# Kernel optimization log

Hardware: AMD Instinct MI355X
Metric: run time of the kernel (lower is better)

## Reference

```python
import jax, jax.numpy as jnp
import numpy as np

N = 50000       # nodes per layer
L = 2           # multiplex layers
F_IN = 128
F_OUT = 32
E_L = 800000    # in-layer edges per layer
NEG_SLOPE = 0.2  # LeakyReLU(0.2)


def _merge_edges(edges_per_layer):
    # offset each layer's edges into the global L*N index space
    parts = [edges_per_layer[i] + i * N for i in range(L)]
    all_edges = jnp.concatenate(parts, axis=1)
    dt = all_edges.dtype
    # self loops on every (layer, node)
    self_loops = jnp.tile(jnp.arange(L * N, dtype=dt)[None, :], (2, 1))
    all_edges = jnp.concatenate([all_edges, self_loops], axis=1)
    # interlayer loops: torch.combinations(arange(L), r=2) + flip([0,1])
    pairs = np.array([(i, j) for i in range(L) for j in range(i + 1, L)], dtype=np.int64)
    pairs = np.concatenate([pairs, pairs[::-1, ::-1]], axis=0)
    all_nodes = np.arange(L * N, dtype=np.int64).reshape(L, N)
    src = all_nodes[pairs[:, 0]].reshape(-1)
    trg = all_nodes[pairs[:, 1]].reshape(-1)
    inter = jnp.asarray(np.stack([src, trg], axis=0)).astype(dt)
    return jnp.concatenate([all_edges, inter], axis=1)  # [2, E_total]


def setup_inputs() -> dict:
    key = jax.random.key(0)
    k1, k2, k3, k4, k5 = jax.random.split(key, 5)
    return {
        "x": jax.random.normal(k1, (1, N, F_IN), dtype=jnp.float32),
        "edge_index0": jax.random.randint(k2, (2, E_L), 0, N, dtype=jnp.int32),
        "edge_index1": jax.random.randint(k3, (2, E_L), 0, N, dtype=jnp.int32),
        "W_proj": jax.random.normal(k4, (L * F_OUT, F_IN), dtype=jnp.float32) * 0.05,
        "W_merge": jax.random.normal(k5, (F_OUT, L * F_OUT), dtype=jnp.float32) * 0.05,
        "bias": jnp.zeros((L, F_OUT), dtype=jnp.float32),
    }


def reference(x, edge_index0, edge_index1, W_proj, W_merge, bias):
    # dropout_prob=0 -> dropout is identity (eval-mode semantics)
    B = x.shape[0]
    edges = _merge_edges([edge_index0, edge_index1])
    src, trg = edges[0], edges[1]
    # degree normalization (naming follows original: in_deg from src, out_deg from trg)
    in_deg = 1.0 / jnp.sqrt(jnp.zeros(L * N, x.dtype).at[src].add(1.0))
    out_deg = 1.0 / jnp.sqrt(jnp.zeros(L * N, x.dtype).at[trg].add(1.0))
    # project F_IN -> L*F_OUT, then split features into L chunks concatenated on node dim
    proj = jnp.einsum('bnf,of->bno', x, W_proj)                 # [B, N, L*F_OUT]
    proj = proj.reshape(B, N, L, F_OUT).transpose(0, 2, 1, 3).reshape(B, L * N, F_OUT)
    proj = proj * out_deg[None, :, None]
    lifted = proj[:, src, :]                                    # [B, E, F_OUT] gather
    agg = jnp.zeros((B, L * N, F_OUT), x.dtype).at[:, trg, :].add(lifted)  # scatter_add
    agg = agg * in_deg[None, :, None]
    out = agg.reshape(B, L, N, F_OUT).transpose(0, 2, 1, 3)     # [B, N, L, F_OUT]
    out = jax.nn.leaky_relu(out + bias, NEG_SLOPE)
    return jnp.einsum('bnk,ok->bno', out.reshape(B, N, L * F_OUT), W_merge)  # [B, N, F_OUT]
```

## Files before the change

kernel.cpp:

```cpp
#include <hip/hip_runtime.h>

#define N_NODES 50000
#define F_IN 128
#define F_OUT 32
#define E_L 800000
#define NEG_SLOPE 0.2f
#define LN 100000
#define NE 1600000
#define BSH 6
#define BNODES 64
#define NB 782
#define CAP 2368
#define PBLOCKS 512
#define PCHUNK 3125
#define CEDGE 7

__global__ __launch_bounds__(512) void partition_kernel(
    const int* __restrict__ e0, const int* __restrict__ e1,
    int* __restrict__ cur_t, int* __restrict__ cur_s,
    int* __restrict__ trgbuf, unsigned char* __restrict__ srcbuf) {
    __shared__ int hist_t[NB], hist_s[NB], res_t[NB], res_s[NB];
    const int t = threadIdx.x, b = blockIdx.x;
    const int l = (b >= PBLOCKS / 2) ? 1 : 0;
    const int* __restrict__ ei = l ? e1 : e0;
    const int ebase = b * PCHUNK - l * E_L;
    for (int i = t; i < NB; i += 512) { hist_t[i] = 0; hist_s[i] = 0; }
    __syncthreads();
    int cs_[CEDGE], ct_[CEDGE];
    #pragma unroll
    for (int j = 0; j < CEDGE; ++j) {
        const int idx = t + j * 512;
        if (idx < PCHUNK) {
            const int e = ebase + idx;
            const int src = ei[e], trg = ei[E_L + e];
            cs_[j] = src; ct_[j] = trg;
            atomicAdd(&hist_t[trg >> BSH], 1);
            atomicAdd(&hist_s[src >> BSH], 1);
        } else { cs_[j] = -1; ct_[j] = -1; }
    }
    __syncthreads();
    for (int i = t; i < NB; i += 512) {
        res_t[i] = hist_t[i] ? atomicAdd(&cur_t[i], hist_t[i]) : 0;
        res_s[i] = hist_s[i] ? atomicAdd(&cur_s[i], hist_s[i]) : 0;
    }
    __syncthreads();
    for (int i = t; i < NB; i += 512) { hist_t[i] = 0; hist_s[i] = 0; }
    __syncthreads();
    #pragma unroll
    for (int j = 0; j < CEDGE; ++j) {
        if (ct_[j] >= 0) {
            const int src = cs_[j], trg = ct_[j];
            const int tb = trg >> BSH, sb = src >> BSH;
            const int st = res_t[tb] + atomicAdd(&hist_t[tb], 1);
            const int ss = res_s[sb] + atomicAdd(&hist_s[sb], 1);
            if (st < CAP)
                trgbuf[tb * CAP + st] =
                    (((l << 6) | (trg & 63)) << 17) | (src + l * N_NODES);
            if (ss < CAP)
                srcbuf[sb * CAP + ss] = (unsigned char)((l << 6) | (src & 63));
        }
    }
}

__global__ __launch_bounds__(256) void count_kernel(
    const int* __restrict__ cur_t, const int* __restrict__ cur_s,
    const int* __restrict__ trgbuf, const unsigned char* __restrict__ srcbuf,
    int* __restrict__ cnt_trg, int* __restrict__ cnt_src) {
    __shared__ int ht[128], hs[128];
    const int t = threadIdx.x, b = blockIdx.x;
    if (t < 128) { ht[t] = 0; hs[t] = 0; }
    __syncthreads();
    const int ct = min(cur_t[b], CAP), cs = min(cur_s[b], CAP);
    for (int i = t; i < ct; i += 256)
        atomicAdd(&ht[(trgbuf[b * CAP + i] >> 17) & 127], 1);
    for (int i = t; i < cs; i += 256)
        atomicAdd(&hs[srcbuf[b * CAP + i] & 127], 1);
    __syncthreads();
    if (t < 128) {
        const int l = t >> 6, n = b * BNODES + (t & 63);
        if (n < N_NODES) {
            cnt_trg[l * N_NODES + n] = ht[t];
            cnt_src[l * N_NODES + n] = hs[t];
        }
    }
}

__global__ __launch_bounds__(256) void proj_kernel(
    const float* __restrict__ x, const float* __restrict__ Wp,
    const int* __restrict__ cnt_trg, float* __restrict__ scaled) {
    __shared__ float Wtt[64][132];
    __shared__ float xt[8][F_IN];
    const int t = threadIdx.x;
    for (int i = t; i < 64 * F_IN; i += 256) {
        int o = i >> 7, k = i & 127;
        Wtt[o][k] = Wp[i];
    }
    const int lane = t & 63, w = t >> 6;
    const int ntiles = N_NODES / 8;
    for (int tile = blockIdx.x; tile < ntiles; tile += gridDim.x) {
        const int base = tile * 8;
        __syncthreads();
        ((float4*)&xt[0][0])[t] = ((const float4*)(x + (size_t)base * F_IN))[t];
        __syncthreads();
        const int n0 = w, n1 = w + 4;
        float acc0 = 0.f, acc1 = 0.f;
        #pragma unroll
        for (int k = 0; k < F_IN; k += 4) {
            float4 wv = *(const float4*)&Wtt[lane][k];
            float4 x0 = *(const float4*)&xt[n0][k];
            float4 x1 = *(const float4*)&xt[n1][k];
            acc0 += wv.x * x0.x + wv.y * x0.y + wv.z * x0.z + wv.w * x0.w;
            acc1 += wv.x * x1.x + wv.y * x1.y + wv.z * x1.z + wv.w * x1.w;
        }
        const int l = lane >> 5, f = lane & 31;
        {
            const int v = l * N_NODES + base + n0;
            const float od = 1.0f / sqrtf((float)(cnt_trg[v] + 2));
            scaled[(size_t)v * F_OUT + f] = acc0 * od;
        }
        {
            const int v = l * N_NODES + base + n1;
            const float od = 1.0f / sqrtf((float)(cnt_trg[v] + 2));
            scaled[(size_t)v * F_OUT + f] = acc1 * od;
        }
    }
}

__global__ __launch_bounds__(512) void mega_kernel(
    const int* __restrict__ cur_t, const int* __restrict__ trgbuf,
    const int* __restrict__ cnt_trg, const int* __restrict__ cnt_src,
    const float* __restrict__ scaled, const float* __restrict__ Wm,
    const float* __restrict__ bias, float* __restrict__ out) {
    __shared__ int   colx[CAP];
    __shared__ int   rp[128], rdeg[128], cursor[128], sc[128];
    __shared__ float h[BNODES][64];
    __shared__ float Wt[64][32];
    __shared__ float bs[64];
    const int t = threadIdx.x, b = blockIdx.x;
    for (int i = t; i < 2048; i += 512) Wt[i >> 5][i & 31] = Wm[(i & 31) * 64 + (i >> 5)];
    if (t < 64) bs[t] = bias[t];
    int cnt_r = 0;
    if (t < 128) {
        const int l = t >> 6, n = b * BNODES + (t & 63);
        cnt_r = (n < N_NODES) ? cnt_trg[l * N_NODES + n] : 0;
        rdeg[t] = cnt_r; sc[t] = cnt_r;
    }
    __syncthreads();
    for (int off = 1; off < 128; off <<= 1) {
        int add = (t < 128 && t >= off) ? sc[t - off] : 0;
        __syncthreads();
        if (t < 128) sc[t] += add;
        __syncthreads();
    }
    if (t < 128) { rp[t] = sc[t] - cnt_r; cursor[t] = sc[t] - cnt_r; }
    __syncthreads();
    const int total = min(cur_t[b], CAP);
    for (int i = t; i < total; i += 512) {
        const int p = trgbuf[b * CAP + i];
        const int slot = atomicAdd(&cursor[(p >> 17) & 127], 1);
        colx[slot] = p & 0x1FFFF;
    }
    __syncthreads();
    const int nl = t >> 3, f = (t & 7) * 4;
    const int n = b * BNODES + nl;
    if (n < N_NODES) {
        const int s0 = rp[nl],      d0 = rdeg[nl];
        const int s1 = rp[nl + 64], d1 = rdeg[nl + 64];
        float4 acc0 = make_float4(0.f, 0.f, 0.f, 0.f);
        float4 acc1 = make_float4(0.f, 0.f, 0.f, 0.f);
        const int m = (d0 > d1) ? d0 : d1;
        #pragma unroll 2
        for (int i = 0; i < m; ++i) {
            if (i < d0) {
                const int u = colx[s0 + i];
                const float4 g = *(const float4*)(scaled + (size_t)u * F_OUT + f);
                acc0.x += g.x; acc0.y += g.y; acc0.z += g.z; acc0.w += g.w;
            }
            if (i < d1) {
                const int u = colx[s1 + i];
                const float4 g = *(const float4*)(scaled + (size_t)u * F_OUT + f);
                acc1.x += g.x; acc1.y += g.y; acc1.z += g.z; acc1.w += g.w;
            }
        }
        const int v = n, vp = N_NODES + n;
        const float4 sv = *(const float4*)(scaled + (size_t)v  * F_OUT + f);
        const float4 pv = *(const float4*)(scaled + (size_t)vp * F_OUT + f);
        const float id0 = rsqrtf((float)(cnt_src[v]  + 2));
        const float id1 = rsqrtf((float)(cnt_src[vp] + 2));
        float4 h0, h1;
        h0.x = (acc0.x + sv.x + pv.x) * id0 + bs[f + 0];
        h0.y = (acc0.y + sv.y + pv.y) * id0 + bs[f + 1];
        h0.z = (acc0.z + sv.z + pv.z) * id0 + bs[f + 2];
        h0.w = (acc0.w + sv.w + pv.w) * id0 + bs[f + 3];
        h1.x = (acc1.x + sv.x + pv.x) * id1 + bs[32 + f + 0];
        h1.y = (acc1.y + sv.y + pv.y) * id1 + bs[32 + f + 1];
        h1.z = (acc1.z + sv.z + pv.z) * id1 + bs[32 + f + 2];
        h1.w = (acc1.w + sv.w + pv.w) * id1 + bs[32 + f + 3];
        h0.x = (h0.x >= 0.f) ? h0.x : NEG_SLOPE * h0.x;
        h0.y = (h0.y >= 0.f) ? h0.y : NEG_SLOPE * h0.y;
        h0.z = (h0.z >= 0.f) ? h0.z : NEG_SLOPE * h0.z;
        h0.w = (h0.w >= 0.f) ? h0.w : NEG_SLOPE * h0.w;
        h1.x = (h1.x >= 0.f) ? h1.x : NEG_SLOPE * h1.x;
        h1.y = (h1.y >= 0.f) ? h1.y : NEG_SLOPE * h1.y;
        h1.z = (h1.z >= 0.f) ? h1.z : NEG_SLOPE * h1.z;
        h1.w = (h1.w >= 0.f) ? h1.w : NEG_SLOPE * h1.w;
        *(float4*)&h[nl][f]      = h0;
        *(float4*)&h[nl][32 + f] = h1;
    }
    __syncthreads();
    for (int i = t; i < BNODES * 32; i += 512) {
        const int nl2 = i >> 5, o = i & 31, n2 = b * BNODES + nl2;
        if (n2 < N_NODES) {
            float acc = 0.f;
            #pragma unroll
            for (int k = 0; k < 64; ++k)
                acc += h[nl2][k] * Wt[k][o];
            out[(size_t)n2 * F_OUT + o] = acc;
        }
    }
}

extern "C" void kernel_launch(void* const* d_in, const int* in_sizes, int n_in,
                              void* d_out, int out_size, void* d_ws, size_t ws_size,
                              hipStream_t stream) {
    const float* x    = (const float*)d_in[0];
    const int*   e0   = (const int*)d_in[1];
    const int*   e1   = (const int*)d_in[2];
    const float* Wp   = (const float*)d_in[3];
    const float* Wm   = (const float*)d_in[4];
    const float* bias = (const float*)d_in[5];
    float* out = (float*)d_out;

    float* scaled = (float*)d_ws;
    unsigned char* srcbuf = (unsigned char*)d_ws;
    int* trgbuf  = (int*)((char*)d_ws + (size_t)LN * F_OUT * sizeof(float));
    int* cur_t   = trgbuf + (size_t)NB * CAP;
    int* cur_s   = cur_t + NB;
    int* cnt_trg = cur_s + NB;
    int* cnt_src = cnt_trg + LN;

    hipMemsetAsync(cur_t, 0, 2 * NB * sizeof(int), stream);

    partition_kernel<<<PBLOCKS, 512, 0, stream>>>(e0, e1, cur_t, cur_s,
                                                  trgbuf, srcbuf);
    count_kernel<<<NB, 256, 0, stream>>>(cur_t, cur_s, trgbuf, srcbuf,
                                         cnt_trg, cnt_src);
    proj_kernel<<<1024, 256, 0, stream>>>(x, Wp, cnt_trg, scaled);
    mega_kernel<<<NB, 512, 0, stream>>>(cur_t, trgbuf, cnt_trg, cnt_src,
                                        scaled, Wm, bias, out);
}
```

Before: 203.3 us.

## Fold degree counting into partition via global atomics and drop count kernel

Removes the separate count kernel and the source-side bucketing buffer. Per-node in/out degrees are now counted directly in the partition kernel with global atomicAdds, and the within-block slot offset from the first histogram pass is reused, so the second shared-atomic pass goes away. The partition grid is halved so each block handles twice the edges. This trades a kernel launch and extra buffer traffic for 3.2M scattered global atomics and a larger memset.

```diff
diff --git a/kernel.cpp b/kernel.cpp
--- a/kernel.cpp
+++ b/kernel.cpp
@@ -11,76 +11,46 @@
 #define BNODES 64
 #define NB 782
 #define CAP 2368
-#define PBLOCKS 512
-#define PCHUNK 3125
-#define CEDGE 7
+#define PBLOCKS 256
+#define PCHUNK 6250
+#define CEDGE 13
 
 __global__ __launch_bounds__(512) void partition_kernel(
     const int* __restrict__ e0, const int* __restrict__ e1,
-    int* __restrict__ cur_t, int* __restrict__ cur_s,
-    int* __restrict__ trgbuf, unsigned char* __restrict__ srcbuf) {
-    __shared__ int hist_t[NB], hist_s[NB], res_t[NB], res_s[NB];
+    int* __restrict__ cur_t, int* __restrict__ trgbuf,
+    int* __restrict__ cnt_trg, int* __restrict__ cnt_src) {
+    __shared__ int hist_t[NB], res_t[NB];
     const int t = threadIdx.x, b = blockIdx.x;
     const int l = (b >= PBLOCKS / 2) ? 1 : 0;
     const int* __restrict__ ei = l ? e1 : e0;
     const int ebase = b * PCHUNK - l * E_L;
-    for (int i = t; i < NB; i += 512) { hist_t[i] = 0; hist_s[i] = 0; }
-    __syncthreads();
-    int cs_[CEDGE], ct_[CEDGE];
+    for (int i = t; i < NB; i += 512) hist_t[i] = 0;
+    __syncthreads();
+    int cu_[CEDGE], ct_[CEDGE], off_[CEDGE];
     #pragma unroll
     for (int j = 0; j < CEDGE; ++j) {
         const int idx = t + j * 512;
         if (idx < PCHUNK) {
             const int e = ebase + idx;
             const int src = ei[e], trg = ei[E_L + e];
-            cs_[j] = src; ct_[j] = trg;
-            atomicAdd(&hist_t[trg >> BSH], 1);
-            atomicAdd(&hist_s[src >> BSH], 1);
-        } else { cs_[j] = -1; ct_[j] = -1; }
-    }
-    __syncthreads();
-    for (int i = t; i < NB; i += 512) {
+            cu_[j] = src; ct_[j] = trg;
+            off_[j] = atomicAdd(&hist_t[trg >> BSH], 1);
+            atomicAdd(&cnt_trg[l * N_NODES + trg], 1);
+            atomicAdd(&cnt_src[l * N_NODES + src], 1);
+        } else { ct_[j] = -1; off_[j] = 0; cu_[j] = 0; }
+    }
+    __syncthreads();
+    for (int i = t; i < NB; i += 512)
         res_t[i] = hist_t[i] ? atomicAdd(&cur_t[i], hist_t[i]) : 0;
-        res_s[i] = hist_s[i] ? atomicAdd(&cur_s[i], hist_s[i]) : 0;
-    }
-    __syncthreads();
-    for (int i = t; i < NB; i += 512) { hist_t[i] = 0; hist_s[i] = 0; }
     __syncthreads();
     #pragma unroll
     for (int j = 0; j < CEDGE; ++j) {
         if (ct_[j] >= 0) {
-            const int src = cs_[j], trg = ct_[j];
-            const int tb = trg >> BSH, sb = src >> BSH;
-            const int st = res_t[tb] + atomicAdd(&hist_t[tb], 1);
-            const int ss = res_s[sb] + atomicAdd(&hist_s[sb], 1);
+            const int trg = ct_[j], tb = trg >> BSH;
+            const int st = res_t[tb] + off_[j];
             if (st < CAP)
                 trgbuf[tb * CAP + st] =
-                    (((l << 6) | (trg & 63)) << 17) | (src + l * N_NODES);
-            if (ss < CAP)
-                srcbuf[sb * CAP + ss] = (unsigned char)((l << 6) | (src & 63));
-        }
-    }
-}
-
-__global__ __launch_bounds__(256) void count_kernel(
-    const int* __restrict__ cur_t, const int* __restrict__ cur_s,
-    const int* __restrict__ trgbuf, const unsigned char* __restrict__ srcbuf,
-    int* __restrict__ cnt_trg, int* __restrict__ cnt_src) {
-    __shared__ int ht[128], hs[128];
-    const int t = threadIdx.x, b = blockIdx.x;
-    if (t < 128) { ht[t] = 0; hs[t] = 0; }
-    __syncthreads();
-    const int ct = min(cur_t[b], CAP), cs = min(cur_s[b], CAP);
-    for (int i = t; i < ct; i += 256)
-        atomicAdd(&ht[(trgbuf[b * CAP + i] >> 17) & 127], 1);
-    for (int i = t; i < cs; i += 256)
-        atomicAdd(&hs[srcbuf[b * CAP + i] & 127], 1);
-    __syncthreads();
-    if (t < 128) {
-        const int l = t >> 6, n = b * BNODES + (t & 63);
-        if (n < N_NODES) {
-            cnt_trg[l * N_NODES + n] = ht[t];
-            cnt_src[l * N_NODES + n] = hs[t];
+                    (((l << 6) | (trg & 63)) << 17) | (cu_[j] + l * N_NODES);
         }
     }
 }
@@ -231,20 +201,16 @@
     const float* bias = (const float*)d_in[5];
     float* out = (float*)d_out;
 
-    float* scaled = (float*)d_ws;
-    unsigned char* srcbuf = (unsigned char*)d_ws;
+    float* scaled  = (float*)d_ws;
     int* trgbuf  = (int*)((char*)d_ws + (size_t)LN * F_OUT * sizeof(float));
     int* cur_t   = trgbuf + (size_t)NB * CAP;
-    int* cur_s   = cur_t + NB;
-    int* cnt_trg = cur_s + NB;
+    int* cnt_trg = cur_t + NB;
     int* cnt_src = cnt_trg + LN;
 
-    hipMemsetAsync(cur_t, 0, 2 * NB * sizeof(int), stream);
-
-    partition_kernel<<<PBLOCKS, 512, 0, stream>>>(e0, e1, cur_t, cur_s,
-                                                  trgbuf, srcbuf);
-    count_kernel<<<NB, 256, 0, stream>>>(cur_t, cur_s, trgbuf, srcbuf,
-                                         cnt_trg, cnt_src);
+    hipMemsetAsync(cur_t, 0, (size_t)(NB + 2 * LN) * sizeof(int), stream);
+
+    partition_kernel<<<PBLOCKS, 512, 0, stream>>>(e0, e1, cur_t, trgbuf,
+                                                  cnt_trg, cnt_src);
     proj_kernel<<<1024, 256, 0, stream>>>(x, Wp, cnt_trg, scaled);
     mega_kernel<<<NB, 512, 0, stream>>>(cur_t, trgbuf, cnt_trg, cnt_src,
                                         scaled, Wm, bias, out);
```

After: 286.1 us. 1.41x slower.
